# Performance work log

Hardware: AMD Instinct MI355X
Metric: run time of the kernel (lower is better)

## Reference

```python
import jax, jax.numpy as jnp
import numpy as np

TOPK = 10

def setup_inputs() -> dict:
    key = jax.random.key(0)
    k1, k2, k3, k4, k5 = jax.random.split(key, 5)
    B, N, M, d = 256, 64, 64, 32
    return {
        "featureVec": jax.random.normal(k1, (B, N, d), dtype=jnp.float32),
        "contextVec": jax.random.normal(k2, (B, M, d), dtype=jnp.float32),
        "Wq": jax.random.normal(k3, (d, d), dtype=jnp.float32) * 0.05,
        "Wk": jax.random.normal(k4, (d, d), dtype=jnp.float32) * 0.05,
        "Wv": jax.random.normal(k5, (d, M), dtype=jnp.float32) * 0.05,
    }


def _lambda_weight(featureVec, contextVec, Wq, Wk, Wv):
    # Lambda-attention producing weight [B, N, M] (M = contextFeatureNum).
    Q = jnp.einsum("bnd,dk->bnk", featureVec, Wq)                 # [B,N,k]
    K = jax.nn.softmax(jnp.einsum("bmd,dk->bmk", contextVec, Wk), axis=1)
    V = jnp.einsum("bmd,dv->bmv", contextVec, Wv)                 # [B,M,v=M]
    lam = jnp.einsum("bmk,bmv->bkv", K, V)                        # content lambda
    return jnp.einsum("bnk,bkv->bnv", Q, lam)                     # [B,N,M]


def reference(featureVec, contextVec, Wq, Wk, Wv):
    B, N, d = featureVec.shape
    # Outer-product value tensor [B, N, M, d]
    value = featureVec[:, :, None, :] * contextVec[:, None, :, :]
    weight = _lambda_weight(featureVec, contextVec, Wq, Wk, Wv)   # [B,N,M]
    topk_vals, idx = jax.lax.top_k(weight, TOPK)                  # [B,N,topk]
    topk_vals = jax.nn.softmax(topk_vals, axis=2)
    # Gather selected context slots along dim 2, then weighted combine.
    out = jnp.take_along_axis(value, idx[..., None], axis=2)      # [B,N,topk,d]
    out = topk_vals[..., None] * out
    return out.reshape(B, N * TOPK, d)
```

## Files before the change

kernel.cpp:

```cpp
#include <hip/hip_runtime.h>
#include <math.h>

constexpr int Bn = 256;
constexpr int Nn = 64;
constexpr int Mn = 64;
constexpr int Dn = 32;
constexpr int TK = 10;
constexpr int NT = 1024;
constexpr int PAD = 68;

__device__ __forceinline__ float exp_np(float x) {
    return (float)exp((double)x);
}
__device__ __forceinline__ unsigned int f2u(float f) {
    unsigned int b = __float_as_uint(f);
    return (b & 0x80000000u) ? ~b : (b | 0x80000000u);
}
__device__ __forceinline__ float u2f(unsigned int u) {
    return __uint_as_float((u & 0x80000000u) ? (u ^ 0x80000000u) : ~u);
}

__global__ __launch_bounds__(NT) void sparse_lambda_attn_kernel(
    const float* __restrict__ fv,
    const float* __restrict__ cv,
    const float* __restrict__ Wq,
    const float* __restrict__ Wk,
    const float* __restrict__ Wv,
    float* __restrict__ out)
{
    #pragma clang fp contract(off)

    __shared__ float f_lds[Nn][Dn];
    __shared__ float c_lds[Mn][Dn];
    __shared__ float fT[Dn][Nn];
    __shared__ float cT[Dn][Mn];
    __shared__ float KpT[Dn][PAD];
    __shared__ float QmT[Dn][PAD];
    __shared__ float Vw[Mn][PAD];
    __shared__ float lamS[Dn][PAD];
    __shared__ float Wt[Nn][PAD];
    __shared__ float colmax[Dn], colsum[Dn];
    __shared__ float topw[Nn][TK];
    __shared__ int   topi[Nn][TK];

    const int b    = blockIdx.x;
    const int tid  = threadIdx.x;
    const int lane = tid & 63;
    const int wid  = tid >> 6;

    if (tid < 512) {
        const float4 v = reinterpret_cast<const float4*>(fv + (size_t)b * Nn * Dn)[tid];
        const int n = tid >> 3, d4 = (tid & 7) << 2;
        *reinterpret_cast<float4*>(&f_lds[n][d4]) = v;
        fT[d4 + 0][n] = v.x; fT[d4 + 1][n] = v.y; fT[d4 + 2][n] = v.z; fT[d4 + 3][n] = v.w;
    } else {
        const int t = tid - 512;
        const float4 v = reinterpret_cast<const float4*>(cv + (size_t)b * Mn * Dn)[t];
        const int m = t >> 3, d4 = (t & 7) << 2;
        *reinterpret_cast<float4*>(&c_lds[m][d4]) = v;
        cT[d4 + 0][m] = v.x; cT[d4 + 1][m] = v.y; cT[d4 + 2][m] = v.z; cT[d4 + 3][m] = v.w;
    }
    __syncthreads();

    if (wid < 8) {
        const int kq = __builtin_amdgcn_readfirstlane(wid);
        const int m = lane;
        const float* wkq = Wk + (kq << 2);
        const float* wvq = Wv + (kq << 3);
        float a0=0.f,a1=0.f,a2=0.f,a3=0.f;
        float b0=0.f,b1=0.f,b2=0.f,b3=0.f,b4=0.f,b5=0.f,b6=0.f,b7=0.f;
        #pragma unroll 4
        for (int d = 0; d < Dn; ++d) {
            const float cc = cT[d][m];
            const float* wr = wkq + d * Dn;
            const float* ur = wvq + d * Mn;
            const float w0 = wr[0], w1 = wr[1], w2 = wr[2], w3 = wr[3];
            const float u0 = ur[0], u1 = ur[1], u2 = ur[2], u3 = ur[3];
            const float u4 = ur[4], u5 = ur[5], u6 = ur[6], u7 = ur[7];
            a0 = a0 + cc * w0;  a1 = a1 + cc * w1;  a2 = a2 + cc * w2;  a3 = a3 + cc * w3;
            b0 = b0 + cc * u0;  b1 = b1 + cc * u1;  b2 = b2 + cc * u2;  b3 = b3 + cc * u3;
            b4 = b4 + cc * u4;  b5 = b5 + cc * u5;  b6 = b6 + cc * u6;  b7 = b7 + cc * u7;
        }
        KpT[(kq << 2) + 0][m] = a0;
        KpT[(kq << 2) + 1][m] = a1;
        KpT[(kq << 2) + 2][m] = a2;
        KpT[(kq << 2) + 3][m] = a3;
        float m0=a0, m1=a1, m2=a2, m3=a3;
        #pragma unroll
        for (int off = 1; off < 64; off <<= 1) {
            m0 = fmaxf(m0, __shfl_xor(m0, off));
            m1 = fmaxf(m1, __shfl_xor(m1, off));
            m2 = fmaxf(m2, __shfl_xor(m2, off));
            m3 = fmaxf(m3, __shfl_xor(m3, off));
        }
        if (lane == 0) {
            colmax[(kq << 2) + 0] = m0;
            colmax[(kq << 2) + 1] = m1;
            colmax[(kq << 2) + 2] = m2;
            colmax[(kq << 2) + 3] = m3;
        }
        float4 r0; r0.x = b0; r0.y = b1; r0.z = b2; r0.w = b3;
        float4 r1; r1.x = b4; r1.y = b5; r1.z = b6; r1.w = b7;
        *reinterpret_cast<float4*>(&Vw[m][(kq << 3) + 0]) = r0;
        *reinterpret_cast<float4*>(&Vw[m][(kq << 3) + 4]) = r1;
    } else {
        const int qq = __builtin_amdgcn_readfirstlane(wid - 8);
        const int n = lane;
        const float* wqq = Wq + (qq << 2);
        float a0=0.f,a1=0.f,a2=0.f,a3=0.f;
        #pragma unroll 4
        for (int d = 0; d < Dn; ++d) {
            const float ff = fT[d][n];
            const float* wr = wqq + d * Dn;
            const float w0 = wr[0], w1 = wr[1], w2 = wr[2], w3 = wr[3];
            a0 = a0 + ff * w0;  a1 = a1 + ff * w1;  a2 = a2 + ff * w2;  a3 = a3 + ff * w3;
        }
        QmT[(qq << 2) + 0][n] = a0;
        QmT[(qq << 2) + 1][n] = a1;
        QmT[(qq << 2) + 2][n] = a2;
        QmT[(qq << 2) + 3][n] = a3;
    }
    __syncthreads();

    for (int i = tid; i < Dn * Mn; i += NT) {
        const int k = i >> 6, m = i & 63;
        KpT[k][m] = exp_np(KpT[k][m] - colmax[k]);
    }
    __syncthreads();
    if (tid < Dn) {
        const int k = tid;
        float s = 0.f;
        for (int m = 0; m < Mn; ++m) s = s + KpT[k][m];
        colsum[k] = s;
    }
    __syncthreads();
    for (int i = tid; i < Dn * Mn; i += NT) {
        const int k = i >> 6, m = i & 63;
        KpT[k][m] = KpT[k][m] / colsum[k];
    }
    __syncthreads();

    if (tid < 128) {
        const int kb = (tid >> 4) << 2;
        const int v4 = (tid & 15) << 2;
        float a00=0.f,a01=0.f,a02=0.f,a03=0.f;
        float a10=0.f,a11=0.f,a12=0.f,a13=0.f;
        float a20=0.f,a21=0.f,a22=0.f,a23=0.f;
        float a30=0.f,a31=0.f,a32=0.f,a33=0.f;
        for (int m = 0; m < Mn; ++m) {
            const float k0 = KpT[kb + 0][m];
            const float k1 = KpT[kb + 1][m];
            const float k2 = KpT[kb + 2][m];
            const float k3 = KpT[kb + 3][m];
            const float4 vv = *reinterpret_cast<const float4*>(&Vw[m][v4]);
            a00 = a00 + k0 * vv.x;  a01 = a01 + k0 * vv.y;  a02 = a02 + k0 * vv.z;  a03 = a03 + k0 * vv.w;
            a10 = a10 + k1 * vv.x;  a11 = a11 + k1 * vv.y;  a12 = a12 + k1 * vv.z;  a13 = a13 + k1 * vv.w;
            a20 = a20 + k2 * vv.x;  a21 = a21 + k2 * vv.y;  a22 = a22 + k2 * vv.z;  a23 = a23 + k2 * vv.w;
            a30 = a30 + k3 * vv.x;  a31 = a31 + k3 * vv.y;  a32 = a32 + k3 * vv.z;  a33 = a33 + k3 * vv.w;
        }
        float4 r;
        r.x=a00; r.y=a01; r.z=a02; r.w=a03; *reinterpret_cast<float4*>(&lamS[kb+0][v4]) = r;
        r.x=a10; r.y=a11; r.z=a12; r.w=a13; *reinterpret_cast<float4*>(&lamS[kb+1][v4]) = r;
        r.x=a20; r.y=a21; r.z=a22; r.w=a23; *reinterpret_cast<float4*>(&lamS[kb+2][v4]) = r;
        r.x=a30; r.y=a31; r.z=a32; r.w=a33; *reinterpret_cast<float4*>(&lamS[kb+3][v4]) = r;
    }
    __syncthreads();

    if (tid < 256) {
        const int nb = (tid >> 4) << 2;
        const int v4 = (tid & 15) << 2;
        float a00=0.f,a01=0.f,a02=0.f,a03=0.f;
        float a10=0.f,a11=0.f,a12=0.f,a13=0.f;
        float a20=0.f,a21=0.f,a22=0.f,a23=0.f;
        float a30=0.f,a31=0.f,a32=0.f,a33=0.f;
        for (int k = 0; k < Dn; ++k) {
            const float q0 = QmT[k][nb + 0];
            const float q1 = QmT[k][nb + 1];
            const float q2 = QmT[k][nb + 2];
            const float q3 = QmT[k][nb + 3];
            const float4 lv = *reinterpret_cast<const float4*>(&lamS[k][v4]);
            a00 = a00 + q0 * lv.x;  a01 = a01 + q0 * lv.y;  a02 = a02 + q0 * lv.z;  a03 = a03 + q0 * lv.w;
            a10 = a10 + q1 * lv.x;  a11 = a11 + q1 * lv.y;  a12 = a12 + q1 * lv.z;  a13 = a13 + q1 * lv.w;
            a20 = a20 + q2 * lv.x;  a21 = a21 + q2 * lv.y;  a22 = a22 + q2 * lv.z;  a23 = a23 + q2 * lv.w;
            a30 = a30 + q3 * lv.x;  a31 = a31 + q3 * lv.y;  a32 = a32 + q3 * lv.z;  a33 = a33 + q3 * lv.w;
        }
        float4 r;
        r.x=a00; r.y=a01; r.z=a02; r.w=a03; *reinterpret_cast<float4*>(&Wt[nb+0][v4]) = r;
        r.x=a10; r.y=a11; r.z=a12; r.w=a13; *reinterpret_cast<float4*>(&Wt[nb+1][v4]) = r;
        r.x=a20; r.y=a21; r.z=a22; r.w=a23; *reinterpret_cast<float4*>(&Wt[nb+2][v4]) = r;
        r.x=a30; r.y=a31; r.z=a32; r.w=a33; *reinterpret_cast<float4*>(&Wt[nb+3][v4]) = r;
    }
    __syncthreads();

    {
        const int g = tid & 15;
        const int n = tid >> 4;

        const float4 s4 = *reinterpret_cast<const float4*>(&Wt[n][g << 2]);
        unsigned su0 = f2u(s4.x), su1 = f2u(s4.y), su2 = f2u(s4.z), su3 = f2u(s4.w);
        unsigned avail = 0xFu;

        float val0 = 0.f, myval = 0.f;
        int   myidx = 0;

        #pragma unroll
        for (int t = 0; t < TK; ++t) {
            unsigned bu = 0u; int bm = 64;
            if ((avail & 1u) && su0 > bu) { bu = su0; bm = (g << 2) + 0; }
            if ((avail & 2u) && su1 > bu) { bu = su1; bm = (g << 2) + 1; }
            if ((avail & 4u) && su2 > bu) { bu = su2; bm = (g << 2) + 2; }
            if ((avail & 8u) && su3 > bu) { bu = su3; bm = (g << 2) + 3; }
            #pragma unroll
            for (int off = 1; off <= 8; off <<= 1) {
                const unsigned ou = __shfl_xor(bu, off);
                const int      om = __shfl_xor(bm, off);
                if (ou > bu || (ou == bu && om < bm)) { bu = ou; bm = om; }
            }
            const float bv = u2f(bu);
            if (t == 0) val0 = bv;
            if (g == t) { myval = bv; myidx = bm; }
            if ((bm >> 2) == g) avail &= ~(1u << (bm & 3));
        }

        const float ev_own = (g < TK) ? exp_np(myval - val0) : 0.f;
        float s = 0.f;
        #pragma unroll
        for (int t = 0; t < TK; ++t) {
            const float e = __shfl(ev_own, (lane & 48) + t);
            s = s + e;
        }
        if (g < TK) {
            topw[n][g] = ev_own / s;
            topi[n][g] = myidx;
        }
    }
    __syncthreads();

    float* ob = out + (size_t)b * (Nn * TK * Dn);
    constexpr int TOT4 = Nn * TK * Dn / 4;
    for (int i = tid; i < TOT4; i += NT) {
        const int n = i / (TK * Dn / 4);
        const int r = i - n * (TK * Dn / 4);
        const int t = r >> 3;
        const int d4 = r & 7;
        const float w = topw[n][t];
        const int m = topi[n][t];
        const float4 f4 = reinterpret_cast<const float4*>(&f_lds[n][0])[d4];
        const float4 c4 = reinterpret_cast<const float4*>(&c_lds[m][0])[d4];
        float4 o;
        { const float vx = f4.x * c4.x; o.x = w * vx; }
        { const float vy = f4.y * c4.y; o.y = w * vy; }
        { const float vz = f4.z * c4.z; o.z = w * vz; }
        { const float vw = f4.w * c4.w; o.w = w * vw; }
        reinterpret_cast<float4*>(ob)[i] = o;
    }
}

extern "C" void kernel_launch(void* const* d_in, const int* in_sizes, int n_in,
                              void* d_out, int out_size, void* d_ws, size_t ws_size,
                              hipStream_t stream) {
    const float* fv = (const float*)d_in[0];
    const float* cv = (const float*)d_in[1];
    const float* Wq = (const float*)d_in[2];
    const float* Wk = (const float*)d_in[3];
    const float* Wv = (const float*)d_in[4];
    float* out = (float*)d_out;

    sparse_lambda_attn_kernel<<<Bn, NT, 0, stream>>>(fv, cv, Wq, Wk, Wv, out);
}
```

Baseline: 26.22 us.

## Fuse key softmax into projection warps and rebalance GEMM work across threads

```diff
diff --git a/kernel.cpp b/kernel.cpp
--- a/kernel.cpp
+++ b/kernel.cpp
@@ -7,7 +7,6 @@
 constexpr int Dn = 32;
 constexpr int TK = 10;
 constexpr int NT = 1024;
-constexpr int PAD = 68;
 
 __device__ __forceinline__ float exp_np(float x) {
     return (float)exp((double)x);
@@ -30,16 +29,13 @@
 {
     #pragma clang fp contract(off)
 
-    __shared__ float f_lds[Nn][Dn];
-    __shared__ float c_lds[Mn][Dn];
-    __shared__ float fT[Dn][Nn];
-    __shared__ float cT[Dn][Mn];
-    __shared__ float KpT[Dn][PAD];
-    __shared__ float QmT[Dn][PAD];
-    __shared__ float Vw[Mn][PAD];
-    __shared__ float lamS[Dn][PAD];
-    __shared__ float Wt[Nn][PAD];
-    __shared__ float colmax[Dn], colsum[Dn];
+    __shared__ float fT[Dn][65];
+    __shared__ float cT[Dn][65];
+    __shared__ float c_lds[Mn][36];
+    __shared__ float KpT[Dn][68];
+    __shared__ float QmT[Dn][68];
+    __shared__ float VwS[Mn][68];
+    __shared__ float lamS[Dn][68];
     __shared__ float topw[Nn][TK];
     __shared__ int   topi[Nn][TK];
 
@@ -51,7 +47,6 @@
     if (tid < 512) {
         const float4 v = reinterpret_cast<const float4*>(fv + (size_t)b * Nn * Dn)[tid];
         const int n = tid >> 3, d4 = (tid & 7) << 2;
-        *reinterpret_cast<float4*>(&f_lds[n][d4]) = v;
         fT[d4 + 0][n] = v.x; fT[d4 + 1][n] = v.y; fT[d4 + 2][n] = v.z; fT[d4 + 3][n] = v.w;
     } else {
         const int t = tid - 512;
@@ -66,26 +61,15 @@
         const int kq = __builtin_amdgcn_readfirstlane(wid);
         const int m = lane;
         const float* wkq = Wk + (kq << 2);
-        const float* wvq = Wv + (kq << 3);
-        float a0=0.f,a1=0.f,a2=0.f,a3=0.f;
-        float b0=0.f,b1=0.f,b2=0.f,b3=0.f,b4=0.f,b5=0.f,b6=0.f,b7=0.f;
+        float a0 = 0.f, a1 = 0.f, a2 = 0.f, a3 = 0.f;
         #pragma unroll 4
         for (int d = 0; d < Dn; ++d) {
             const float cc = cT[d][m];
             const float* wr = wkq + d * Dn;
-            const float* ur = wvq + d * Mn;
             const float w0 = wr[0], w1 = wr[1], w2 = wr[2], w3 = wr[3];
-            const float u0 = ur[0], u1 = ur[1], u2 = ur[2], u3 = ur[3];
-            const float u4 = ur[4], u5 = ur[5], u6 = ur[6], u7 = ur[7];
             a0 = a0 + cc * w0;  a1 = a1 + cc * w1;  a2 = a2 + cc * w2;  a3 = a3 + cc * w3;
-            b0 = b0 + cc * u0;  b1 = b1 + cc * u1;  b2 = b2 + cc * u2;  b3 = b3 + cc * u3;
-            b4 = b4 + cc * u4;  b5 = b5 + cc * u5;  b6 = b6 + cc * u6;  b7 = b7 + cc * u7;
-        }
-        KpT[(kq << 2) + 0][m] = a0;
-        KpT[(kq << 2) + 1][m] = a1;
-        KpT[(kq << 2) + 2][m] = a2;
-        KpT[(kq << 2) + 3][m] = a3;
-        float m0=a0, m1=a1, m2=a2, m3=a3;
+        }
+        float m0 = a0, m1 = a1, m2 = a2, m3 = a3;
         #pragma unroll
         for (int off = 1; off < 64; off <<= 1) {
             m0 = fmaxf(m0, __shfl_xor(m0, off));
@@ -93,102 +77,76 @@
             m2 = fmaxf(m2, __shfl_xor(m2, off));
             m3 = fmaxf(m3, __shfl_xor(m3, off));
         }
-        if (lane == 0) {
-            colmax[(kq << 2) + 0] = m0;
-            colmax[(kq << 2) + 1] = m1;
-            colmax[(kq << 2) + 2] = m2;
-            colmax[(kq << 2) + 3] = m3;
-        }
+        const float e0 = exp_np(a0 - m0);
+        const float e1 = exp_np(a1 - m1);
+        const float e2 = exp_np(a2 - m2);
+        const float e3 = exp_np(a3 - m3);
+        float s0 = 0.f, s1 = 0.f, s2 = 0.f, s3 = 0.f;
+        #pragma unroll
+        for (int t = 0; t < 64; ++t) {
+            s0 = s0 + __shfl(e0, t);
+            s1 = s1 + __shfl(e1, t);
+            s2 = s2 + __shfl(e2, t);
+            s3 = s3 + __shfl(e3, t);
+        }
+        KpT[(kq << 2) + 0][m] = e0 / s0;
+        KpT[(kq << 2) + 1][m] = e1 / s1;
+        KpT[(kq << 2) + 2][m] = e2 / s2;
+        KpT[(kq << 2) + 3][m] = e3 / s3;
+    } else {
+        const int q = __builtin_amdgcn_readfirstlane(wid - 8);
+        const int nm = lane;
+        const float* wqq = Wq + (q << 2);
+        const float* wvq = Wv + (q << 3);
+        float a0 = 0.f, a1 = 0.f, a2 = 0.f, a3 = 0.f;
+        float b0 = 0.f, b1 = 0.f, b2 = 0.f, b3 = 0.f, b4 = 0.f, b5 = 0.f, b6 = 0.f, b7 = 0.f;
+        #pragma unroll 4
+        for (int d = 0; d < Dn; ++d) {
+            const float ff = fT[d][nm];
+            const float cc = cT[d][nm];
+            const float* wr = wqq + d * Dn;
+            const float* ur = wvq + d * Mn;
+            const float w0 = wr[0], w1 = wr[1], w2 = wr[2], w3 = wr[3];
+            const float u0 = ur[0], u1 = ur[1], u2 = ur[2], u3 = ur[3];
+            const float u4 = ur[4], u5 = ur[5], u6 = ur[6], u7 = ur[7];
+            a0 = a0 + ff * w0;  a1 = a1 + ff * w1;  a2 = a2 + ff * w2;  a3 = a3 + ff * w3;
+            b0 = b0 + cc * u0;  b1 = b1 + cc * u1;  b2 = b2 + cc * u2;  b3 = b3 + cc * u3;
+            b4 = b4 + cc * u4;  b5 = b5 + cc * u5;  b6 = b6 + cc * u6;  b7 = b7 + cc * u7;
+        }
+        QmT[(q << 2) + 0][nm] = a0;
+        QmT[(q << 2) + 1][nm] = a1;
+        QmT[(q << 2) + 2][nm] = a2;
+        QmT[(q << 2) + 3][nm] = a3;
         float4 r0; r0.x = b0; r0.y = b1; r0.z = b2; r0.w = b3;
         float4 r1; r1.x = b4; r1.y = b5; r1.z = b6; r1.w = b7;
-        *reinterpret_cast<float4*>(&Vw[m][(kq << 3) + 0]) = r0;
-        *reinterpret_cast<float4*>(&Vw[m][(kq << 3) + 4]) = r1;
-    } else {
-        const int qq = __builtin_amdgcn_readfirstlane(wid - 8);
-        const int n = lane;
-        const float* wqq = Wq + (qq << 2);
-        float a0=0.f,a1=0.f,a2=0.f,a3=0.f;
-        #pragma unroll 4
-        for (int d = 0; d < Dn; ++d) {
-            const float ff = fT[d][n];
-            const float* wr = wqq + d * Dn;
-            const float w0 = wr[0], w1 = wr[1], w2 = wr[2], w3 = wr[3];
-            a0 = a0 + ff * w0;  a1 = a1 + ff * w1;  a2 = a2 + ff * w2;  a3 = a3 + ff * w3;
-        }
-        QmT[(qq << 2) + 0][n] = a0;
-        QmT[(qq << 2) + 1][n] = a1;
-        QmT[(qq << 2) + 2][n] = a2;
-        QmT[(qq << 2) + 3][n] = a3;
-    }
-    __syncthreads();
-
-    for (int i = tid; i < Dn * Mn; i += NT) {
-        const int k = i >> 6, m = i & 63;
-        KpT[k][m] = exp_np(KpT[k][m] - colmax[k]);
-    }
-    __syncthreads();
-    if (tid < Dn) {
-        const int k = tid;
-        float s = 0.f;
-        for (int m = 0; m < Mn; ++m) s = s + KpT[k][m];
-        colsum[k] = s;
-    }
-    __syncthreads();
-    for (int i = tid; i < Dn * Mn; i += NT) {
-        const int k = i >> 6, m = i & 63;
-        KpT[k][m] = KpT[k][m] / colsum[k];
-    }
-    __syncthreads();
-
-    if (tid < 128) {
-        const int kb = (tid >> 4) << 2;
-        const int v4 = (tid & 15) << 2;
-        float a00=0.f,a01=0.f,a02=0.f,a03=0.f;
-        float a10=0.f,a11=0.f,a12=0.f,a13=0.f;
-        float a20=0.f,a21=0.f,a22=0.f,a23=0.f;
-        float a30=0.f,a31=0.f,a32=0.f,a33=0.f;
+        *reinterpret_cast<float4*>(&VwS[nm][(q << 3) + 0]) = r0;
+        *reinterpret_cast<float4*>(&VwS[nm][(q << 3) + 4]) = r1;
+    }
+    __syncthreads();
+
+    if (tid < 512) {
+        const int k = tid >> 4, v4 = (tid & 15) << 2;
+        float a0 = 0.f, a1 = 0.f, a2 = 0.f, a3 = 0.f;
         for (int m = 0; m < Mn; ++m) {
-            const float k0 = KpT[kb + 0][m];
-            const float k1 = KpT[kb + 1][m];
-            const float k2 = KpT[kb + 2][m];
-            const float k3 = KpT[kb + 3][m];
-            const float4 vv = *reinterpret_cast<const float4*>(&Vw[m][v4]);
-            a00 = a00 + k0 * vv.x;  a01 = a01 + k0 * vv.y;  a02 = a02 + k0 * vv.z;  a03 = a03 + k0 * vv.w;
-            a10 = a10 + k1 * vv.x;  a11 = a11 + k1 * vv.y;  a12 = a12 + k1 * vv.z;  a13 = a13 + k1 * vv.w;
-            a20 = a20 + k2 * vv.x;  a21 = a21 + k2 * vv.y;  a22 = a22 + k2 * vv.z;  a23 = a23 + k2 * vv.w;
-            a30 = a30 + k3 * vv.x;  a31 = a31 + k3 * vv.y;  a32 = a32 + k3 * vv.z;  a33 = a33 + k3 * vv.w;
-        }
-        float4 r;
-        r.x=a00; r.y=a01; r.z=a02; r.w=a03; *reinterpret_cast<float4*>(&lamS[kb+0][v4]) = r;
-        r.x=a10; r.y=a11; r.z=a12; r.w=a13; *reinterpret_cast<float4*>(&lamS[kb+1][v4]) = r;
-        r.x=a20; r.y=a21; r.z=a22; r.w=a23; *reinterpret_cast<float4*>(&lamS[kb+2][v4]) = r;
-        r.x=a30; r.y=a31; r.z=a32; r.w=a33; *reinterpret_cast<float4*>(&lamS[kb+3][v4]) = r;
-    }
-    __syncthreads();
-
-    if (tid < 256) {
-        const int nb = (tid >> 4) << 2;
-        const int v4 = (tid & 15) << 2;
-        float a00=0.f,a01=0.f,a02=0.f,a03=0.f;
-        float a10=0.f,a11=0.f,a12=0.f,a13=0.f;
-        float a20=0.f,a21=0.f,a22=0.f,a23=0.f;
-        float a30=0.f,a31=0.f,a32=0.f,a33=0.f;
+            const float kk = KpT[k][m];
+            const float4 vv = *reinterpret_cast<const float4*>(&VwS[m][v4]);
+            a0 = a0 + kk * vv.x;  a1 = a1 + kk * vv.y;  a2 = a2 + kk * vv.z;  a3 = a3 + kk * vv.w;
+        }
+        float4 r; r.x = a0; r.y = a1; r.z = a2; r.w = a3;
+        *reinterpret_cast<float4*>(&lamS[k][v4]) = r;
+    }
+    __syncthreads();
+
+    {
+        const int n = tid >> 4, v4 = (tid & 15) << 2;
+        float a0 = 0.f, a1 = 0.f, a2 = 0.f, a3 = 0.f;
         for (int k = 0; k < Dn; ++k) {
-            const float q0 = QmT[k][nb + 0];
-            const float q1 = QmT[k][nb + 1];
-            const float q2 = QmT[k][nb + 2];
-            const float q3 = QmT[k][nb + 3];
+            const float qq = QmT[k][n];
             const float4 lv = *reinterpret_cast<const float4*>(&lamS[k][v4]);
-            a00 = a00 + q0 * lv.x;  a01 = a01 + q0 * lv.y;  a02 = a02 + q0 * lv.z;  a03 = a03 + q0 * lv.w;
-            a10 = a10 + q1 * lv.x;  a11 = a11 + q1 * lv.y;  a12 = a12 + q1 * lv.z;  a13 = a13 + q1 * lv.w;
-            a20 = a20 + q2 * lv.x;  a21 = a21 + q2 * lv.y;  a22 = a22 + q2 * lv.z;  a23 = a23 + q2 * lv.w;
-            a30 = a30 + q3 * lv.x;  a31 = a31 + q3 * lv.y;  a32 = a32 + q3 * lv.z;  a33 = a33 + q3 * lv.w;
-        }
-        float4 r;
-        r.x=a00; r.y=a01; r.z=a02; r.w=a03; *reinterpret_cast<float4*>(&Wt[nb+0][v4]) = r;
-        r.x=a10; r.y=a11; r.z=a12; r.w=a13; *reinterpret_cast<float4*>(&Wt[nb+1][v4]) = r;
-        r.x=a20; r.y=a21; r.z=a22; r.w=a23; *reinterpret_cast<float4*>(&Wt[nb+2][v4]) = r;
-        r.x=a30; r.y=a31; r.z=a32; r.w=a33; *reinterpret_cast<float4*>(&Wt[nb+3][v4]) = r;
+            a0 = a0 + qq * lv.x;  a1 = a1 + qq * lv.y;  a2 = a2 + qq * lv.z;  a3 = a3 + qq * lv.w;
+        }
+        float4 r; r.x = a0; r.y = a1; r.z = a2; r.w = a3;
+        *reinterpret_cast<float4*>(&VwS[n][v4]) = r;
     }
     __syncthreads();
 
@@ -196,7 +154,7 @@
         const int g = tid & 15;
         const int n = tid >> 4;
 
-        const float4 s4 = *reinterpret_cast<const float4*>(&Wt[n][g << 2]);
+        const float4 s4 = *reinterpret_cast<const float4*>(&VwS[n][g << 2]);
         unsigned su0 = f2u(s4.x), su1 = f2u(s4.y), su2 = f2u(s4.z), su3 = f2u(s4.w);
         unsigned avail = 0xFu;
 
@@ -242,16 +200,19 @@
         const int n = i / (TK * Dn / 4);
         const int r = i - n * (TK * Dn / 4);
         const int t = r >> 3;
-        const int d4 = r & 7;
+        const int d4 = (r & 7) << 2;
         const float w = topw[n][t];
         const int m = topi[n][t];
-        const float4 f4 = reinterpret_cast<const float4*>(&f_lds[n][0])[d4];
-        const float4 c4 = reinterpret_cast<const float4*>(&c_lds[m][0])[d4];
+        const float f0 = fT[d4 + 0][n];
+        const float f1 = fT[d4 + 1][n];
+        const float f2 = fT[d4 + 2][n];
+        const float f3 = fT[d4 + 3][n];
+        const float4 c4 = *reinterpret_cast<const float4*>(&c_lds[m][d4]);
         float4 o;
-        { const float vx = f4.x * c4.x; o.x = w * vx; }
-        { const float vy = f4.y * c4.y; o.y = w * vy; }
-        { const float vz = f4.z * c4.z; o.z = w * vz; }
-        { const float vw = f4.w * c4.w; o.w = w * vw; }
+        { const float vx = f0 * c4.x; o.x = w * vx; }
+        { const float vy = f1 * c4.y; o.y = w * vy; }
+        { const float vz = f2 * c4.z; o.z = w * vz; }
+        { const float vw = f3 * c4.w; o.w = w * vw; }
         reinterpret_cast<float4*>(ob)[i] = o;
     }
 }
```

Result: slower. 27.55 us (+5.1%).
